# Optimization experiments

Hardware: AMD Instinct MI355X
Metric: run time of the kernel (lower is better)

The kernel has to match this reference:

```python
import jax, jax.numpy as jnp
import numpy as np

B, NMAX, H, Q, S = 4096, 64, 768, 16384, 256
TEMP = 0.1  # infonce_temperature default


def setup_inputs() -> dict:
    key = jax.random.key(0)
    ks = jax.random.split(key, 8)
    padded = jax.random.normal(ks[0], (B, NMAX, H), jnp.float32)
    lengths = jax.random.randint(ks[1], (B,), 1, NMAX + 1)  # every node has >=1 token
    query_w = jax.random.normal(ks[2], (H,), jnp.float32) * 0.02
    query_b = jnp.zeros((1,), jnp.float32)
    wm_w = jax.random.normal(ks[3], (2 * H,), jnp.float32) * 0.02
    wm_b = jnp.zeros((1,), jnp.float32)
    node_predict_indexs = jax.random.randint(ks[4], (Q,), 0, B)
    change_node_indexs = jax.random.randint(ks[5], (S,), 0, B)
    node_predict_types = jax.random.randint(ks[6], (Q,), 0, S)
    node_predict_labels = jax.random.randint(ks[7], (Q, 1), 0, 2)
    return dict(padded=padded, query_w=query_w, query_b=query_b, wm_w=wm_w, wm_b=wm_b,
                lengths=lengths, node_predict_indexs=node_predict_indexs,
                change_node_indexs=change_node_indexs, node_predict_types=node_predict_types,
                node_predict_labels=node_predict_labels)


def _forward(padded, query_w, query_b, wm_w, wm_b, lengths,
             node_predict_indexs, change_node_indexs, node_predict_types, node_predict_labels):
    # merge(): attention-pool each padded ragged sequence -> [B, H]
    scores = jnp.einsum('bnh,h->bn', padded, query_w) + query_b[0]      # [B, NMAX]
    mask = jnp.arange(NMAX)[None, :] < lengths[:, None]                  # [B, NMAX]
    scores = jnp.where(mask, scores, -jnp.inf)
    weights = jax.nn.softmax(scores, axis=1)
    node_emb = jnp.einsum('bnh,bn->bh', padded, weights)                 # [B, H]

    # loss_fn_infonce(), vectorized over all types via segment ops
    tgt = node_emb[node_predict_indexs]                                  # [Q, H]
    src = node_emb[change_node_indexs][node_predict_types]               # [Q, H] (per-type source)
    sims = jnp.concatenate([src, tgt], axis=1) @ wm_w + wm_b[0]          # [Q] (w_metric)
    logits = sims / TEMP

    types = node_predict_types
    pos = node_predict_labels[:, 0] == 1

    gmax = jax.ops.segment_max(logits, types, num_segments=S)
    gmax_s = jnp.where(jnp.isfinite(gmax), gmax, 0.0)
    sum_all = jax.ops.segment_sum(jnp.exp(logits - gmax_s[types]), types, num_segments=S)

    pos_logits = jnp.where(pos, logits, -jnp.inf)
    pmax = jax.ops.segment_max(pos_logits, types, num_segments=S)
    pmax_s = jnp.where(jnp.isfinite(pmax), pmax, 0.0)
    sum_pos = jax.ops.segment_sum(jnp.where(pos, jnp.exp(logits - pmax_s[types]), 0.0),
                                  types, num_segments=S)

    has_pos = jax.ops.segment_sum(pos.astype(jnp.float32), types, num_segments=S) > 0
    lse_all = jnp.log(jnp.where(has_pos, sum_all, 1.0)) + gmax_s
    lse_pos = jnp.log(jnp.where(has_pos, sum_pos, 1.0)) + pmax_s
    n_valid = jnp.maximum(jnp.sum(has_pos.astype(jnp.float32)), 1.0)
    loss = jnp.sum(jnp.where(has_pos, lse_all - lse_pos, 0.0)) / n_valid
    return loss


def reference(padded, query_w, query_b, wm_w, wm_b, lengths,
              node_predict_indexs, change_node_indexs, node_predict_types, node_predict_labels):
    return _forward(padded, query_w, query_b, wm_w, wm_b, lengths,
                    node_predict_indexs, change_node_indexs, node_predict_types, node_predict_labels)
```

## Files before the change

### kernel.cpp

```cpp
#include <hip/hip_runtime.h>
#include <math.h>

#define B_SZ   4096
#define NMAX_SZ 64
#define H_SZ   768
#define Q_SZ   16384
#define S_SZ   256

typedef float f4 __attribute__((ext_vector_type(4)));

__device__ __forceinline__ f4 ldnt(const float* p) {
  return __builtin_nontemporal_load((const f4*)p);
}
__device__ __forceinline__ float dot4(const f4 a, const f4 b) {
  const f4 p = a * b;
  return p[0] + p[1] + p[2] + p[3];
}

__global__ __launch_bounds__(256, 4) void merge_dots_kernel(
    const float* __restrict__ padded, const float* __restrict__ qw,
    const float* __restrict__ wmw, const int* __restrict__ lengths,
    float* __restrict__ d1, float* __restrict__ d2) {
  const int b = blockIdx.x;
  const int t = threadIdx.x;
  const int lane = t & 63;
  const int w = t >> 6;
  const int len = lengths[b];
  const int o0 = 4 * lane;
  const int o1 = 256 + 4 * lane;
  const int o2 = 512 + 4 * lane;
  const float LOG2E = 1.4426950408889634f;

  __shared__ float sl[4];
  __shared__ float sa[12 * 4 * 64];

  f4 q0 = *(const f4*)(qw + o0) * LOG2E;
  f4 q1 = *(const f4*)(qw + o1) * LOG2E;
  f4 q2 = *(const f4*)(qw + o2) * LOG2E;

  const int lo = (len * w) >> 2;
  const int hi = (len * (w + 1)) >> 2;
  const int cnt = hi - lo;
  const float* wbase = padded + (size_t)b * (NMAX_SZ * H_SZ) + (size_t)lo * H_SZ;

  float l = 0.f;
  f4 a0 = {0, 0, 0, 0}, a1 = {0, 0, 0, 0}, a2 = {0, 0, 0, 0};

  if (cnt > 0) {
    const float* rA = wbase;
    const float* rB = wbase + (size_t)((1 < cnt) ? 1 : 0) * H_SZ;
    f4 xA0 = ldnt(rA + o0), xA1 = ldnt(rA + o1), xA2 = ldnt(rA + o2);
    f4 xB0 = ldnt(rB + o0), xB1 = ldnt(rB + o1), xB2 = ldnt(rB + o2);

    for (int k = 0; k < cnt; k += 2) {
      const int pA = (k + 2 < cnt) ? k + 2 : cnt - 1;
      const int pB = (k + 3 < cnt) ? k + 3 : cnt - 1;
      const float* fA = wbase + (size_t)pA * H_SZ;
      const float* fB = wbase + (size_t)pB * H_SZ;
      const f4 nA0 = ldnt(fA + o0), nA1 = ldnt(fA + o1), nA2 = ldnt(fA + o2);
      const f4 nB0 = ldnt(fB + o0), nB1 = ldnt(fB + o1), nB2 = ldnt(fB + o2);

      float pa = dot4(xA0, q0) + dot4(xA1, q1) + dot4(xA2, q2);
      float pb = dot4(xB0, q0) + dot4(xB1, q1) + dot4(xB2, q2);
#pragma unroll
      for (int off = 32; off > 0; off >>= 1) {
        pa += __shfl_xor(pa, off);
        pb += __shfl_xor(pb, off);
      }

      const float eA = exp2f(pa);
      const float eB = (k + 1 < cnt) ? exp2f(pb) : 0.f;
      l += eA + eB;
      a0 += eA * xA0 + eB * xB0;
      a1 += eA * xA1 + eB * xB1;
      a2 += eA * xA2 + eB * xB2;

      xA0 = nA0; xA1 = nA1; xA2 = nA2;
      xB0 = nB0; xB1 = nB1; xB2 = nB2;
    }
  }

  if (lane == 0) sl[w] = l;
  if (w != 0) {
    const float av[12] = {a0[0], a0[1], a0[2], a0[3], a1[0], a1[1], a1[2], a1[3],
                          a2[0], a2[1], a2[2], a2[3]};
#pragma unroll
    for (int i = 0; i < 12; ++i) sa[i * 256 + w * 64 + lane] = av[i];
  }
  __syncthreads();
  if (w != 0) return;

  const float L = sl[0] + sl[1] + sl[2] + sl[3];
  const float inv = 1.f / L;

  float e[12] = {a0[0], a0[1], a0[2], a0[3], a1[0], a1[1], a1[2], a1[3],
                 a2[0], a2[1], a2[2], a2[3]};
#pragma unroll
  for (int i = 0; i < 12; ++i) {
    e[i] = (e[i] + sa[i * 256 + 64 + lane] +
            sa[i * 256 + 128 + lane] + sa[i * 256 + 192 + lane]) * inv;
  }

  const f4 w10 = *(const f4*)(wmw + o0);
  const f4 w11 = *(const f4*)(wmw + o1);
  const f4 w12 = *(const f4*)(wmw + o2);
  const f4 w20 = *(const f4*)(wmw + H_SZ + o0);
  const f4 w21 = *(const f4*)(wmw + H_SZ + o1);
  const f4 w22 = *(const f4*)(wmw + H_SZ + o2);
  float p1 = e[0] * w10[0] + e[1] * w10[1] + e[2] * w10[2] + e[3] * w10[3]
           + e[4] * w11[0] + e[5] * w11[1] + e[6] * w11[2] + e[7] * w11[3]
           + e[8] * w12[0] + e[9] * w12[1] + e[10] * w12[2] + e[11] * w12[3];
  float p2 = e[0] * w20[0] + e[1] * w20[1] + e[2] * w20[2] + e[3] * w20[3]
           + e[4] * w21[0] + e[5] * w21[1] + e[6] * w21[2] + e[7] * w21[3]
           + e[8] * w22[0] + e[9] * w22[1] + e[10] * w22[2] + e[11] * w22[3];
#pragma unroll
  for (int off = 32; off > 0; off >>= 1) {
    p1 += __shfl_xor(p1, off);
    p2 += __shfl_xor(p2, off);
  }
  if (lane == 0) {
    d1[b] = p1;
    d2[b] = p2;
  }
}

__global__ __launch_bounds__(256) void segment_kernel(
    const float* __restrict__ d1, const float* __restrict__ d2,
    const float* __restrict__ wmb,
    const int* __restrict__ npi, const int* __restrict__ cni,
    const int* __restrict__ npt, const int* __restrict__ labels,
    float* __restrict__ seg_term, float* __restrict__ seg_has) {
  const int s = blockIdx.x;
  const int t = threadIdx.x;
  const int lane = t & 63, wid = t >> 6;
  __shared__ float rg[4], rp[4], sa4[4], sp4[4], cp4[4];

  const float base = d1[cni[s]] + wmb[0];

  float gmax = -INFINITY, pmax = -INFINITY;
  for (int q = t; q < Q_SZ; q += 256) {
    if (npt[q] == s) {
      const float lg = (base + d2[npi[q]]) * 10.f;
      gmax = fmaxf(gmax, lg);
      if (labels[q] == 1) pmax = fmaxf(pmax, lg);
    }
  }
#pragma unroll
  for (int off = 32; off > 0; off >>= 1) {
    gmax = fmaxf(gmax, __shfl_xor(gmax, off));
    pmax = fmaxf(pmax, __shfl_xor(pmax, off));
  }
  if (lane == 0) { rg[wid] = gmax; rp[wid] = pmax; }
  __syncthreads();
  gmax = fmaxf(fmaxf(rg[0], rg[1]), fmaxf(rg[2], rg[3]));
  pmax = fmaxf(fmaxf(rp[0], rp[1]), fmaxf(rp[2], rp[3]));
  const float gmaxs = (gmax == -INFINITY) ? 0.f : gmax;
  const float pmaxs = (pmax == -INFINITY) ? 0.f : pmax;

  float sa = 0.f, sp = 0.f, cnt = 0.f;
  for (int q = t; q < Q_SZ; q += 256) {
    if (npt[q] == s) {
      const float lg = (base + d2[npi[q]]) * 10.f;
      sa += expf(lg - gmaxs);
      if (labels[q] == 1) { sp += expf(lg - pmaxs); cnt += 1.f; }
    }
  }
#pragma unroll
  for (int off = 32; off > 0; off >>= 1) {
    sa += __shfl_xor(sa, off);
    sp += __shfl_xor(sp, off);
    cnt += __shfl_xor(cnt, off);
  }
  if (lane == 0) { sa4[wid] = sa; sp4[wid] = sp; cp4[wid] = cnt; }
  __syncthreads();
  if (t == 0) {
    sa = sa4[0] + sa4[1] + sa4[2] + sa4[3];
    sp = sp4[0] + sp4[1] + sp4[2] + sp4[3];
    cnt = cp4[0] + cp4[1] + cp4[2] + cp4[3];
    const bool haspos = cnt > 0.f;
    float term = 0.f;
    if (haspos) term = (logf(sa) + gmaxs) - (logf(sp) + pmaxs);
    seg_term[s] = term;
    seg_has[s] = haspos ? 1.f : 0.f;
  }
}

__global__ __launch_bounds__(256) void finalize_kernel(
    const float* __restrict__ seg_term, const float* __restrict__ seg_has,
    float* __restrict__ out) {
  const int t = threadIdx.x;
  const int lane = t & 63, wid = t >> 6;
  __shared__ float rt[4], rh[4];
  float v = seg_term[t];
  float h = seg_has[t];
#pragma unroll
  for (int off = 32; off > 0; off >>= 1) {
    v += __shfl_xor(v, off);
    h += __shfl_xor(h, off);
  }
  if (lane == 0) { rt[wid] = v; rh[wid] = h; }
  __syncthreads();
  if (t == 0) {
    const float total = rt[0] + rt[1] + rt[2] + rt[3];
    const float nv = rh[0] + rh[1] + rh[2] + rh[3];
    out[0] = total / fmaxf(nv, 1.f);
  }
}

extern "C" void kernel_launch(void* const* d_in, const int* in_sizes, int n_in,
                              void* d_out, int out_size, void* d_ws, size_t ws_size,
                              hipStream_t stream) {
  const float* padded  = (const float*)d_in[0];
  const float* qw      = (const float*)d_in[1];
  const float* wmw     = (const float*)d_in[3];
  const float* wmb     = (const float*)d_in[4];
  const int*   lengths = (const int*)d_in[5];
  const int*   npi     = (const int*)d_in[6];
  const int*   cni     = (const int*)d_in[7];
  const int*   npt     = (const int*)d_in[8];
  const int*   labels  = (const int*)d_in[9];
  float* out = (float*)d_out;

  float* d1       = (float*)d_ws;
  float* d2       = d1 + B_SZ;
  float* seg_term = d2 + B_SZ;
  float* seg_has  = seg_term + S_SZ;

  merge_dots_kernel<<<B_SZ, 256, 0, stream>>>(padded, qw, wmw, lengths, d1, d2);
  segment_kernel<<<S_SZ, 256, 0, stream>>>(d1, d2, wmb, npi, cni, npt, labels,
                                           seg_term, seg_has);
  finalize_kernel<<<1, 256, 0, stream>>>(seg_term, seg_has, out);
}
```

Before: 99.32 us.

## Project tokens onto metric weights per token instead of pooling embeddings first

Reorders the algebra so that each token row is dotted with both halves of the metric weight vector inside the streaming loop. Only softmax-weighted scalars (U, V, l) are accumulated, so the 768-wide pooled embedding is never built. This removes the 12-float-per-lane shared-memory cross-wave reduction and the separate final projection. In exchange, each token now needs three dot products and six wave shuffle reductions instead of one dot and two, which adds ALU and cross-lane work to a loop that is mostly memory-bound.

```diff
diff --git a/kernel.cpp b/kernel.cpp
--- a/kernel.cpp
+++ b/kernel.cpp
@@ -31,20 +31,24 @@
   const int o2 = 512 + 4 * lane;
   const float LOG2E = 1.4426950408889634f;
 
-  __shared__ float sl[4];
-  __shared__ float sa[12 * 4 * 64];
-
-  f4 q0 = *(const f4*)(qw + o0) * LOG2E;
-  f4 q1 = *(const f4*)(qw + o1) * LOG2E;
-  f4 q2 = *(const f4*)(qw + o2) * LOG2E;
+  __shared__ float sU[4], sV[4], sL[4];
+
+  const f4 g0 = *(const f4*)(qw + o0) * LOG2E;
+  const f4 g1 = *(const f4*)(qw + o1) * LOG2E;
+  const f4 g2 = *(const f4*)(qw + o2) * LOG2E;
+  const f4 u0 = *(const f4*)(wmw + o0);
+  const f4 u1 = *(const f4*)(wmw + o1);
+  const f4 u2 = *(const f4*)(wmw + o2);
+  const f4 v0 = *(const f4*)(wmw + H_SZ + o0);
+  const f4 v1 = *(const f4*)(wmw + H_SZ + o1);
+  const f4 v2 = *(const f4*)(wmw + H_SZ + o2);
 
   const int lo = (len * w) >> 2;
   const int hi = (len * (w + 1)) >> 2;
   const int cnt = hi - lo;
   const float* wbase = padded + (size_t)b * (NMAX_SZ * H_SZ) + (size_t)lo * H_SZ;
 
-  float l = 0.f;
-  f4 a0 = {0, 0, 0, 0}, a1 = {0, 0, 0, 0}, a2 = {0, 0, 0, 0};
+  float U = 0.f, V = 0.f, l = 0.f;
 
   if (cnt > 0) {
     const float* rA = wbase;
@@ -60,67 +64,43 @@
       const f4 nA0 = ldnt(fA + o0), nA1 = ldnt(fA + o1), nA2 = ldnt(fA + o2);
       const f4 nB0 = ldnt(fB + o0), nB1 = ldnt(fB + o1), nB2 = ldnt(fB + o2);
 
-      float pa = dot4(xA0, q0) + dot4(xA1, q1) + dot4(xA2, q2);
-      float pb = dot4(xB0, q0) + dot4(xB1, q1) + dot4(xB2, q2);
+      float sa_ = dot4(xA0, g0) + dot4(xA1, g1) + dot4(xA2, g2);
+      float ua_ = dot4(xA0, u0) + dot4(xA1, u1) + dot4(xA2, u2);
+      float va_ = dot4(xA0, v0) + dot4(xA1, v1) + dot4(xA2, v2);
+      float sb_ = dot4(xB0, g0) + dot4(xB1, g1) + dot4(xB2, g2);
+      float ub_ = dot4(xB0, u0) + dot4(xB1, u1) + dot4(xB2, u2);
+      float vb_ = dot4(xB0, v0) + dot4(xB1, v1) + dot4(xB2, v2);
+
 #pragma unroll
       for (int off = 32; off > 0; off >>= 1) {
-        pa += __shfl_xor(pa, off);
-        pb += __shfl_xor(pb, off);
+        sa_ += __shfl_xor(sa_, off);
+        sb_ += __shfl_xor(sb_, off);
+        ua_ += __shfl_xor(ua_, off);
+        ub_ += __shfl_xor(ub_, off);
+        va_ += __shfl_xor(va_, off);
+        vb_ += __shfl_xor(vb_, off);
       }
 
-      const float eA = exp2f(pa);
-      const float eB = (k + 1 < cnt) ? exp2f(pb) : 0.f;
+      const float eA = exp2f(sa_);
+      const float eB = (k + 1 < cnt) ? exp2f(sb_) : 0.f;
       l += eA + eB;
-      a0 += eA * xA0 + eB * xB0;
-      a1 += eA * xA1 + eB * xB1;
-      a2 += eA * xA2 + eB * xB2;
+      U = fmaf(eA, ua_, fmaf(eB, ub_, U));
+      V = fmaf(eA, va_, fmaf(eB, vb_, V));
 
       xA0 = nA0; xA1 = nA1; xA2 = nA2;
       xB0 = nB0; xB1 = nB1; xB2 = nB2;
     }
   }
 
-  if (lane == 0) sl[w] = l;
-  if (w != 0) {
-    const float av[12] = {a0[0], a0[1], a0[2], a0[3], a1[0], a1[1], a1[2], a1[3],
-                          a2[0], a2[1], a2[2], a2[3]};
-#pragma unroll
-    for (int i = 0; i < 12; ++i) sa[i * 256 + w * 64 + lane] = av[i];
-  }
-  __syncthreads();
-  if (w != 0) return;
-
-  const float L = sl[0] + sl[1] + sl[2] + sl[3];
-  const float inv = 1.f / L;
-
-  float e[12] = {a0[0], a0[1], a0[2], a0[3], a1[0], a1[1], a1[2], a1[3],
-                 a2[0], a2[1], a2[2], a2[3]};
-#pragma unroll
-  for (int i = 0; i < 12; ++i) {
-    e[i] = (e[i] + sa[i * 256 + 64 + lane] +
-            sa[i * 256 + 128 + lane] + sa[i * 256 + 192 + lane]) * inv;
-  }
-
-  const f4 w10 = *(const f4*)(wmw + o0);
-  const f4 w11 = *(const f4*)(wmw + o1);
-  const f4 w12 = *(const f4*)(wmw + o2);
-  const f4 w20 = *(const f4*)(wmw + H_SZ + o0);
-  const f4 w21 = *(const f4*)(wmw + H_SZ + o1);
-  const f4 w22 = *(const f4*)(wmw + H_SZ + o2);
-  float p1 = e[0] * w10[0] + e[1] * w10[1] + e[2] * w10[2] + e[3] * w10[3]
-           + e[4] * w11[0] + e[5] * w11[1] + e[6] * w11[2] + e[7] * w11[3]
-           + e[8] * w12[0] + e[9] * w12[1] + e[10] * w12[2] + e[11] * w12[3];
-  float p2 = e[0] * w20[0] + e[1] * w20[1] + e[2] * w20[2] + e[3] * w20[3]
-           + e[4] * w21[0] + e[5] * w21[1] + e[6] * w21[2] + e[7] * w21[3]
-           + e[8] * w22[0] + e[9] * w22[1] + e[10] * w22[2] + e[11] * w22[3];
-#pragma unroll
-  for (int off = 32; off > 0; off >>= 1) {
-    p1 += __shfl_xor(p1, off);
-    p2 += __shfl_xor(p2, off);
-  }
-  if (lane == 0) {
-    d1[b] = p1;
-    d2[b] = p2;
+  if (lane == 0) { sU[w] = U; sV[w] = V; sL[w] = l; }
+  __syncthreads();
+  if (t == 0) {
+    const float Ut = sU[0] + sU[1] + sU[2] + sU[3];
+    const float Vt = sV[0] + sV[1] + sV[2] + sV[3];
+    const float Lt = sL[0] + sL[1] + sL[2] + sL[3];
+    const float inv = 1.f / Lt;
+    d1[b] = Ut * inv;
+    d2[b] = Vt * inv;
   }
 }
 
```

Result: no change. 100.2 us (+0.9%).
